# Performance work log

Measured on AMD Instinct MI355X. Metric: run time of the kernel, lower is better.

The kernel has to match this reference:

```python
import jax, jax.numpy as jnp
import numpy as np

T = 8192
D_IN = 512
D_QK = 64
D_V = 64


def setup_inputs() -> dict:
    key = jax.random.key(0)
    kx, kq, kk, kv, kl = jax.random.split(key, 5)
    x = jax.random.normal(kx, (T, D_IN), dtype=jnp.float32)
    Wq = jax.random.normal(kq, (D_IN, D_QK), dtype=jnp.float32) * 0.02
    Wk = jax.random.normal(kk, (D_IN, D_QK), dtype=jnp.float32) * 0.02
    Wv = jax.random.normal(kv, (D_IN, D_V), dtype=jnp.float32) * 0.02
    l = jax.random.normal(kl, (T, T), dtype=jnp.float32) * 0.02
    return {"x": x, "Wq": Wq, "Wk": Wk, "Wv": Wv, "l": l}


def reference(x, Wq, Wk, Wv, l):
    # q: [T, d_qk], k: [T, d_qk], v: [T, d_v]
    q = x @ Wq
    k = x @ Wk
    v = x @ Wv
    # scores: [T, S] = (q k^T) elementwise-weighted by learned tril matrix
    scores = jnp.einsum("tn,sn->ts", q, k) * jnp.tril(l)
    # output: [T, d_v]
    return scores @ v
```

## Files before the change

kernel.cpp:

```cpp
#include <hip/hip_runtime.h>
#include <hip/hip_bf16.h>

#define TT 8192
#define DIN 512
#define DQK 64

typedef __attribute__((ext_vector_type(8))) short short8;
typedef __attribute__((ext_vector_type(4))) float f32x4;

__global__ __launch_bounds__(256) void zero_kernel(float* __restrict__ out, int n4)
{
    int i = blockIdx.x * 256 + threadIdx.x;
    if (i < n4) ((f32x4*)out)[i] = (f32x4){0.f, 0.f, 0.f, 0.f};
}

__global__ __launch_bounds__(256) void wconv_kernel(
    const float* __restrict__ Wq, const float* __restrict__ Wk, const float* __restrict__ Wv,
    __hip_bfloat16* __restrict__ wtb)
{
    __shared__ float tile[64][65];
    const int m = blockIdx.y;
    const float* W = m == 0 ? Wq : (m == 1 ? Wk : Wv);
    const int k0 = blockIdx.x * 64;
    const int tid = threadIdx.x;

    {
        const int col4 = (tid & 15) * 4;
        #pragma unroll
        for (int it = 0; it < 4; ++it) {
            const int row = (tid >> 4) + it * 16;
            float4 v = *(const float4*)&W[(size_t)(k0 + row) * DQK + col4];
            tile[row][col4 + 0] = v.x; tile[row][col4 + 1] = v.y;
            tile[row][col4 + 2] = v.z; tile[row][col4 + 3] = v.w;
        }
    }
    __syncthreads();
    {
        const int d = tid >> 2;
        const int kc = (tid & 3) * 16;
        short tmp[16];
        #pragma unroll
        for (int j = 0; j < 16; ++j) {
            __hip_bfloat16 h = __float2bfloat16(tile[kc + j][d]);
            tmp[j] = *(short*)&h;
        }
        short* dst = (short*)wtb + ((size_t)m * 64 + d) * DIN + k0 + kc;
        *(short8*)dst       = *(short8*)&tmp[0];
        *(short8*)(dst + 8) = *(short8*)&tmp[8];
    }
}

#define PP 72

__global__ __launch_bounds__(256) void proj_kernel(
    const float* __restrict__ x,
    const __hip_bfloat16* __restrict__ wtb,
    __hip_bfloat16* __restrict__ qb, __hip_bfloat16* __restrict__ kb,
    __hip_bfloat16* __restrict__ vt)
{
    __shared__ short xb[64][PP];
    __shared__ short wb[3][64][PP];

    const int rowBase = blockIdx.x * 64;
    const int tid = threadIdx.x;
    const int lane = tid & 63;
    const int w = tid >> 6;
    const int lo = lane & 15, hi = lane >> 4;

    f32x4 acc[3][4];
    #pragma unroll
    for (int m = 0; m < 3; ++m)
        #pragma unroll
        for (int cf = 0; cf < 4; ++cf) acc[m][cf] = (f32x4){0.f, 0.f, 0.f, 0.f};

    for (int kk = 0; kk < DIN; kk += 64) {
        {
            const int r = tid >> 2;
            const int c0 = (tid & 3) * 16;
            const float* xp = x + (size_t)(rowBase + r) * DIN + kk + c0;
            short tmp[16];
            #pragma unroll
            for (int j = 0; j < 16; j += 4) {
                float4 v = *(const float4*)(xp + j);
                __hip_bfloat16 h0 = __float2bfloat16(v.x);
                __hip_bfloat16 h1 = __float2bfloat16(v.y);
                __hip_bfloat16 h2 = __float2bfloat16(v.z);
                __hip_bfloat16 h3 = __float2bfloat16(v.w);
                tmp[j + 0] = *(short*)&h0; tmp[j + 1] = *(short*)&h1;
                tmp[j + 2] = *(short*)&h2; tmp[j + 3] = *(short*)&h3;
            }
            *(short8*)&xb[r][c0]     = *(short8*)&tmp[0];
            *(short8*)&xb[r][c0 + 8] = *(short8*)&tmp[8];
        }
        {
            const int d = tid >> 2;
            const int kc = (tid & 3) * 16;
            #pragma unroll
            for (int m = 0; m < 3; ++m) {
                const short* src = (const short*)wtb + ((size_t)m * 64 + d) * DIN + kk + kc;
                *(short8*)&wb[m][d][kc]     = *(const short8*)src;
                *(short8*)&wb[m][d][kc + 8] = *(const short8*)(src + 8);
            }
        }
        __syncthreads();

        short8 a0 = *(short8*)&xb[w * 16 + lo][hi * 8];
        short8 a1 = *(short8*)&xb[w * 16 + lo][32 + hi * 8];
        #pragma unroll
        for (int m = 0; m < 3; ++m) {
            #pragma unroll
            for (int cf = 0; cf < 4; ++cf) {
                short8 b0 = *(short8*)&wb[m][cf * 16 + lo][hi * 8];
                short8 b1 = *(short8*)&wb[m][cf * 16 + lo][32 + hi * 8];
                acc[m][cf] = __builtin_amdgcn_mfma_f32_16x16x32_bf16(a0, b0, acc[m][cf], 0, 0, 0);
                acc[m][cf] = __builtin_amdgcn_mfma_f32_16x16x32_bf16(a1, b1, acc[m][cf], 0, 0, 0);
            }
        }
        __syncthreads();
    }

    #pragma unroll
    for (int cf = 0; cf < 4; ++cf) {
        #pragma unroll
        for (int r = 0; r < 4; ++r) {
            const int tg = rowBase + w * 16 + hi * 4 + r;
            const int d  = cf * 16 + lo;
            __hip_bfloat16 hq = __float2bfloat16(acc[0][cf][r]);
            __hip_bfloat16 hk = __float2bfloat16(acc[1][cf][r]);
            __hip_bfloat16 hv = __float2bfloat16(acc[2][cf][r]);
            qb[(size_t)tg * DQK + d] = hq;
            kb[(size_t)tg * DQK + d] = hk;
            vt[(size_t)d * TT + tg]  = hv;
        }
    }
}

#define TM 128
#define TS 64
#define SCHUNK 512
#define LP 72

__global__ __launch_bounds__(512) void attn_kernel(
    const __hip_bfloat16* __restrict__ qb,
    const __hip_bfloat16* __restrict__ kb,
    const __hip_bfloat16* __restrict__ vt,
    const float* __restrict__ l,
    float* __restrict__ out)
{
    __shared__ short K_lds[2][TS][LP];
    __shared__ short V_lds[2][DQK][LP];
    __shared__ short S_lds[8][16][LP];

    const int t0 = blockIdx.x * TM;
    const int sStart = blockIdx.y * SCHUNK;
    if (sStart >= t0 + TM) return;
    const int sEnd = min(sStart + SCHUNK, t0 + TM);

    const int tid = threadIdx.x;
    const int lane = tid & 63;
    const int w = tid >> 6;
    const int lo = lane & 15, hi = lane >> 4;
    const int trow = t0 + w * 16;
    const int r0 = hi * 4;

    const int srow = tid >> 3;
    const int sc8  = (tid & 7) * 8;

    short8 qf0, qf1;
    {
        const short* qp = (const short*)qb + (size_t)(trow + lo) * DQK;
        qf0 = *(const short8*)(qp + hi * 8);
        qf1 = *(const short8*)(qp + 32 + hi * 8);
    }

    f32x4 acc_o[4];
    #pragma unroll
    for (int i = 0; i < 4; ++i) acc_o[i] = (f32x4){0.f, 0.f, 0.f, 0.f};

    short8 kreg = *(const short8*)((const short*)kb + (size_t)(sStart + srow) * DQK + sc8);
    short8 vreg = *(const short8*)((const short*)vt + (size_t)srow * TT + sStart + sc8);

    float lvC[4][4];
    float lvN[4][4];
    {
        const bool act0 = (sStart <= trow + 15);
        #pragma unroll
        for (int sub = 0; sub < 4; ++sub) {
            const int s_glob = sStart + sub * 16 + lo;
            #pragma unroll
            for (int r = 0; r < 4; ++r) {
                const int tg = trow + r0 + r;
                lvC[sub][r] = (act0 && s_glob <= tg)
                    ? __builtin_nontemporal_load(&l[(size_t)tg * TT + s_glob]) : 0.f;
            }
        }
    }

    *(short8*)&K_lds[0][srow][sc8] = kreg;
    *(short8*)&V_lds[0][srow][sc8] = vreg;
    __syncthreads();

    int cur = 0;
    for (int s0 = sStart; s0 < sEnd; s0 += TS) {
        const int sN = s0 + TS;
        const bool havN = (sN < sEnd);

        if (havN) {
            kreg = *(const short8*)((const short*)kb + (size_t)(sN + srow) * DQK + sc8);
            vreg = *(const short8*)((const short*)vt + (size_t)srow * TT + sN + sc8);
        }

        const bool actN = havN && (sN <= trow + 15);
        if (actN) {
            if (sN + TS - 1 <= trow) {
                #pragma unroll
                for (int sub = 0; sub < 4; ++sub) {
                    const int s_glob = sN + sub * 16 + lo;
                    #pragma unroll
                    for (int r = 0; r < 4; ++r) {
                        const int tg = trow + r0 + r;
                        lvN[sub][r] = __builtin_nontemporal_load(&l[(size_t)tg * TT + s_glob]);
                    }
                }
            } else {
                #pragma unroll
                for (int sub = 0; sub < 4; ++sub) {
                    const int s_glob = sN + sub * 16 + lo;
                    #pragma unroll
                    for (int r = 0; r < 4; ++r) {
                        const int tg = trow + r0 + r;
                        lvN[sub][r] = (s_glob <= tg)
                            ? __builtin_nontemporal_load(&l[(size_t)tg * TT + s_glob]) : 0.f;
                    }
                }
            }
        } else {
            #pragma unroll
            for (int sub = 0; sub < 4; ++sub)
                #pragma unroll
                for (int r = 0; r < 4; ++r) lvN[sub][r] = 0.f;
        }

        if (s0 <= trow + 15) {
            #pragma unroll
            for (int sub = 0; sub < 4; ++sub) {
                f32x4 acc = (f32x4){0.f, 0.f, 0.f, 0.f};
                short8 b0 = *(short8*)&K_lds[cur][sub * 16 + lo][hi * 8];
                short8 b1 = *(short8*)&K_lds[cur][sub * 16 + lo][32 + hi * 8];
                acc = __builtin_amdgcn_mfma_f32_16x16x32_bf16(qf0, b0, acc, 0, 0, 0);
                acc = __builtin_amdgcn_mfma_f32_16x16x32_bf16(qf1, b1, acc, 0, 0, 0);
                #pragma unroll
                for (int r = 0; r < 4; ++r) {
                    float sv = acc[r] * lvC[sub][r];
                    __hip_bfloat16 h = __float2bfloat16(sv);
                    S_lds[w][r0 + r][sub * 16 + lo] = *(short*)&h;
                }
            }
            short8 a0 = *(short8*)&S_lds[w][lo][hi * 8];
            short8 a1 = *(short8*)&S_lds[w][lo][32 + hi * 8];
            #pragma unroll
            for (int ds = 0; ds < 4; ++ds) {
                short8 b0 = *(short8*)&V_lds[cur][ds * 16 + lo][hi * 8];
                short8 b1 = *(short8*)&V_lds[cur][ds * 16 + lo][32 + hi * 8];
                acc_o[ds] = __builtin_amdgcn_mfma_f32_16x16x32_bf16(a0, b0, acc_o[ds], 0, 0, 0);
                acc_o[ds] = __builtin_amdgcn_mfma_f32_16x16x32_bf16(a1, b1, acc_o[ds], 0, 0, 0);
            }
        }

        if (havN) {
            *(short8*)&K_lds[cur ^ 1][srow][sc8] = kreg;
            *(short8*)&V_lds[cur ^ 1][srow][sc8] = vreg;
        }
        __syncthreads();
        cur ^= 1;

        #pragma unroll
        for (int sub = 0; sub < 4; ++sub)
            #pragma unroll
            for (int r = 0; r < 4; ++r)
                lvC[sub][r] = lvN[sub][r];
    }

    #pragma unroll
    for (int ds = 0; ds < 4; ++ds) {
        #pragma unroll
        for (int r = 0; r < 4; ++r) {
            const int tg = trow + r0 + r;
            atomicAdd(&out[(size_t)tg * DQK + ds * 16 + lo], acc_o[ds][r]);
        }
    }
}

extern "C" void kernel_launch(void* const* d_in, const int* in_sizes, int n_in,
                              void* d_out, int out_size, void* d_ws, size_t ws_size,
                              hipStream_t stream) {
    const float* x  = (const float*)d_in[0];
    const float* Wq = (const float*)d_in[1];
    const float* Wk = (const float*)d_in[2];
    const float* Wv = (const float*)d_in[3];
    const float* l  = (const float*)d_in[4];
    float* out = (float*)d_out;

    __hip_bfloat16* qb  = (__hip_bfloat16*)d_ws;
    __hip_bfloat16* kb  = qb + (size_t)TT * DQK;
    __hip_bfloat16* vt  = kb + (size_t)TT * DQK;
    __hip_bfloat16* wtb = vt + (size_t)TT * DQK;

    zero_kernel<<<(out_size / 4 + 255) / 256, 256, 0, stream>>>(out, out_size / 4);
    wconv_kernel<<<dim3(DIN / 64, 3), 256, 0, stream>>>(Wq, Wk, Wv, wtb);
    proj_kernel<<<TT / 64, 256, 0, stream>>>(x, wtb, qb, kb, vt);
    attn_kernel<<<dim3(TT / TM, TT / SCHUNK), 512, 0, stream>>>(qb, kb, vt, l, out);
}
```

Baseline: 82.52 us.

## Vectorize l loads via transposed score MFMA, shuffle scores, rework projection

New measurement: 108.5 us. +31.5%, slower.

```diff
diff --git a/kernel.cpp b/kernel.cpp
--- a/kernel.cpp
+++ b/kernel.cpp
@@ -7,6 +7,25 @@
 
 typedef __attribute__((ext_vector_type(8))) short short8;
 typedef __attribute__((ext_vector_type(4))) float f32x4;
+typedef __attribute__((ext_vector_type(4))) unsigned u32x4;
+
+union S8U4 { u32x4 u; short8 s; };
+
+static __device__ __forceinline__ unsigned pack_bf16(float a, float b) {
+    __hip_bfloat16 ha = __float2bfloat16(a);
+    __hip_bfloat16 hb = __float2bfloat16(b);
+    return (unsigned)(*(unsigned short*)&ha) | ((unsigned)(*(unsigned short*)&hb) << 16);
+}
+
+static __device__ __forceinline__ short8 cvt8(const float* p) {
+    short tmp[8];
+    #pragma unroll
+    for (int j = 0; j < 8; ++j) {
+        __hip_bfloat16 h = __float2bfloat16(p[j]);
+        tmp[j] = *(short*)&h;
+    }
+    return *(short8*)tmp;
+}
 
 __global__ __launch_bounds__(256) void zero_kernel(float* __restrict__ out, int n4)
 {
@@ -50,21 +69,15 @@
     }
 }
 
-#define PP 72
-
-__global__ __launch_bounds__(256) void proj_kernel(
+__global__ __launch_bounds__(64) void proj_kernel(
     const float* __restrict__ x,
     const __hip_bfloat16* __restrict__ wtb,
     __hip_bfloat16* __restrict__ qb, __hip_bfloat16* __restrict__ kb,
     __hip_bfloat16* __restrict__ vt)
 {
-    __shared__ short xb[64][PP];
-    __shared__ short wb[3][64][PP];
-
-    const int rowBase = blockIdx.x * 64;
-    const int tid = threadIdx.x;
-    const int lane = tid & 63;
-    const int w = tid >> 6;
+    __shared__ float tile[16][65];
+    const int rowBase = blockIdx.x * 16;
+    const int lane = threadIdx.x;
     const int lo = lane & 15, hi = lane >> 4;
 
     f32x4 acc[3][4];
@@ -73,71 +86,63 @@
         #pragma unroll
         for (int cf = 0; cf < 4; ++cf) acc[m][cf] = (f32x4){0.f, 0.f, 0.f, 0.f};
 
+    const float* xp0 = x + (size_t)(rowBase + lo) * DIN + hi * 8;
+    const short* wb0 = (const short*)wtb + (size_t)lo * DIN + hi * 8;
+
     for (int kk = 0; kk < DIN; kk += 64) {
-        {
-            const int r = tid >> 2;
-            const int c0 = (tid & 3) * 16;
-            const float* xp = x + (size_t)(rowBase + r) * DIN + kk + c0;
-            short tmp[16];
-            #pragma unroll
-            for (int j = 0; j < 16; j += 4) {
-                float4 v = *(const float4*)(xp + j);
-                __hip_bfloat16 h0 = __float2bfloat16(v.x);
-                __hip_bfloat16 h1 = __float2bfloat16(v.y);
-                __hip_bfloat16 h2 = __float2bfloat16(v.z);
-                __hip_bfloat16 h3 = __float2bfloat16(v.w);
-                tmp[j + 0] = *(short*)&h0; tmp[j + 1] = *(short*)&h1;
-                tmp[j + 2] = *(short*)&h2; tmp[j + 3] = *(short*)&h3;
-            }
-            *(short8*)&xb[r][c0]     = *(short8*)&tmp[0];
-            *(short8*)&xb[r][c0 + 8] = *(short8*)&tmp[8];
-        }
-        {
-            const int d = tid >> 2;
-            const int kc = (tid & 3) * 16;
-            #pragma unroll
-            for (int m = 0; m < 3; ++m) {
-                const short* src = (const short*)wtb + ((size_t)m * 64 + d) * DIN + kk + kc;
-                *(short8*)&wb[m][d][kc]     = *(const short8*)src;
-                *(short8*)&wb[m][d][kc + 8] = *(const short8*)(src + 8);
-            }
-        }
-        __syncthreads();
-
-        short8 a0 = *(short8*)&xb[w * 16 + lo][hi * 8];
-        short8 a1 = *(short8*)&xb[w * 16 + lo][32 + hi * 8];
+        float xa[8], xb[8];
+        *(float4*)&xa[0] = *(const float4*)(xp0 + kk);
+        *(float4*)&xa[4] = *(const float4*)(xp0 + kk + 4);
+        *(float4*)&xb[0] = *(const float4*)(xp0 + kk + 32);
+        *(float4*)&xb[4] = *(const float4*)(xp0 + kk + 36);
+        short8 af0 = cvt8(xa), af1 = cvt8(xb);
         #pragma unroll
         for (int m = 0; m < 3; ++m) {
             #pragma unroll
             for (int cf = 0; cf < 4; ++cf) {
-                short8 b0 = *(short8*)&wb[m][cf * 16 + lo][hi * 8];
-                short8 b1 = *(short8*)&wb[m][cf * 16 + lo][32 + hi * 8];
-                acc[m][cf] = __builtin_amdgcn_mfma_f32_16x16x32_bf16(a0, b0, acc[m][cf], 0, 0, 0);
-                acc[m][cf] = __builtin_amdgcn_mfma_f32_16x16x32_bf16(a1, b1, acc[m][cf], 0, 0, 0);
-            }
-        }
-        __syncthreads();
-    }
-
-    #pragma unroll
-    for (int cf = 0; cf < 4; ++cf) {
-        #pragma unroll
-        for (int r = 0; r < 4; ++r) {
-            const int tg = rowBase + w * 16 + hi * 4 + r;
-            const int d  = cf * 16 + lo;
-            __hip_bfloat16 hq = __float2bfloat16(acc[0][cf][r]);
-            __hip_bfloat16 hk = __float2bfloat16(acc[1][cf][r]);
-            __hip_bfloat16 hv = __float2bfloat16(acc[2][cf][r]);
-            qb[(size_t)tg * DQK + d] = hq;
-            kb[(size_t)tg * DQK + d] = hk;
-            vt[(size_t)d * TT + tg]  = hv;
-        }
+                const short* wp = wb0 + ((size_t)m * 64 + cf * 16) * DIN + kk;
+                short8 b0 = *(const short8*)wp;
+                short8 b1 = *(const short8*)(wp + 32);
+                acc[m][cf] = __builtin_amdgcn_mfma_f32_16x16x32_bf16(af0, b0, acc[m][cf], 0, 0, 0);
+                acc[m][cf] = __builtin_amdgcn_mfma_f32_16x16x32_bf16(af1, b1, acc[m][cf], 0, 0, 0);
+            }
+        }
+    }
+
+    #pragma unroll
+    for (int m = 0; m < 2; ++m) {
+        __hip_bfloat16* o = (m == 0) ? qb : kb;
+        #pragma unroll
+        for (int cf = 0; cf < 4; ++cf)
+            #pragma unroll
+            for (int r = 0; r < 4; ++r)
+                o[(size_t)(rowBase + 4 * hi + r) * DQK + cf * 16 + lo] =
+                    __float2bfloat16(acc[m][cf][r]);
+    }
+
+    #pragma unroll
+    for (int cf = 0; cf < 4; ++cf)
+        #pragma unroll
+        for (int r = 0; r < 4; ++r)
+            tile[4 * hi + r][cf * 16 + lo] = acc[2][cf][r];
+    __syncthreads();
+    {
+        const int d = lane;
+        short tmp[16];
+        #pragma unroll
+        for (int j = 0; j < 16; ++j) {
+            __hip_bfloat16 h = __float2bfloat16(tile[j][d]);
+            tmp[j] = *(short*)&h;
+        }
+        short* dst = (short*)vt + (size_t)d * TT + rowBase;
+        *(short8*)dst       = *(short8*)&tmp[0];
+        *(short8*)(dst + 8) = *(short8*)&tmp[8];
     }
 }
 
 #define TM 128
 #define TS 64
-#define SCHUNK 512
+#define SCHUNK 256
 #define LP 72
 
 __global__ __launch_bounds__(512) void attn_kernel(
@@ -149,7 +154,6 @@
 {
     __shared__ short K_lds[2][TS][LP];
     __shared__ short V_lds[2][DQK][LP];
-    __shared__ short S_lds[8][16][LP];
 
     const int t0 = blockIdx.x * TM;
     const int sStart = blockIdx.y * SCHUNK;
@@ -161,14 +165,14 @@
     const int w = tid >> 6;
     const int lo = lane & 15, hi = lane >> 4;
     const int trow = t0 + w * 16;
-    const int r0 = hi * 4;
+    const int tmine = trow + lo;
 
     const int srow = tid >> 3;
     const int sc8  = (tid & 7) * 8;
 
     short8 qf0, qf1;
     {
-        const short* qp = (const short*)qb + (size_t)(trow + lo) * DQK;
+        const short* qp = (const short*)qb + (size_t)tmine * DQK;
         qf0 = *(const short8*)(qp + hi * 8);
         qf1 = *(const short8*)(qp + 32 + hi * 8);
     }
@@ -177,22 +181,29 @@
     #pragma unroll
     for (int i = 0; i < 4; ++i) acc_o[i] = (f32x4){0.f, 0.f, 0.f, 0.f};
 
+    const float* lrow = l + (size_t)tmine * TT;
+
     short8 kreg = *(const short8*)((const short*)kb + (size_t)(sStart + srow) * DQK + sc8);
     short8 vreg = *(const short8*)((const short*)vt + (size_t)srow * TT + sStart + sc8);
 
     float lvC[4][4];
-    float lvN[4][4];
-    {
-        const bool act0 = (sStart <= trow + 15);
-        #pragma unroll
-        for (int sub = 0; sub < 4; ++sub) {
-            const int s_glob = sStart + sub * 16 + lo;
-            #pragma unroll
-            for (int r = 0; r < 4; ++r) {
-                const int tg = trow + r0 + r;
-                lvC[sub][r] = (act0 && s_glob <= tg)
-                    ? __builtin_nontemporal_load(&l[(size_t)tg * TT + s_glob]) : 0.f;
-            }
+    if (sStart <= trow + 15) {
+        float raw[4][4];
+        #pragma unroll
+        for (int sub = 0; sub < 4; ++sub)
+            *(f32x4*)raw[sub] = __builtin_nontemporal_load(
+                (const f32x4*)(lrow + sStart + sub * 16 + 4 * hi));
+        if (sStart + 63 <= trow) {
+            #pragma unroll
+            for (int sub = 0; sub < 4; ++sub)
+                #pragma unroll
+                for (int r = 0; r < 4; ++r) lvC[sub][r] = raw[sub][r];
+        } else {
+            #pragma unroll
+            for (int sub = 0; sub < 4; ++sub)
+                #pragma unroll
+                for (int r = 0; r < 4; ++r)
+                    lvC[sub][r] = (sStart + sub * 16 + 4 * hi + r <= tmine) ? raw[sub][r] : 0.f;
         }
     }
 
@@ -200,70 +211,63 @@
     *(short8*)&V_lds[0][srow][sc8] = vreg;
     __syncthreads();
 
+    const int nsteps = (sEnd - sStart) / TS;
     int cur = 0;
-    for (int s0 = sStart; s0 < sEnd; s0 += TS) {
+    for (int n = 0; n < nsteps; ++n) {
+        const int s0 = sStart + n * TS;
         const int sN = s0 + TS;
-        const bool havN = (sN < sEnd);
-
+        const bool havN = (n + 1 < nsteps);
+        const bool actN = havN && (sN <= trow + 15);
+
+        float lvN[4][4];
+        if (actN) {
+            #pragma unroll
+            for (int sub = 0; sub < 4; ++sub)
+                *(f32x4*)lvN[sub] = __builtin_nontemporal_load(
+                    (const f32x4*)(lrow + sN + sub * 16 + 4 * hi));
+        }
         if (havN) {
             kreg = *(const short8*)((const short*)kb + (size_t)(sN + srow) * DQK + sc8);
             vreg = *(const short8*)((const short*)vt + (size_t)srow * TT + sN + sc8);
         }
 
-        const bool actN = havN && (sN <= trow + 15);
-        if (actN) {
-            if (sN + TS - 1 <= trow) {
-                #pragma unroll
-                for (int sub = 0; sub < 4; ++sub) {
-                    const int s_glob = sN + sub * 16 + lo;
-                    #pragma unroll
-                    for (int r = 0; r < 4; ++r) {
-                        const int tg = trow + r0 + r;
-                        lvN[sub][r] = __builtin_nontemporal_load(&l[(size_t)tg * TT + s_glob]);
-                    }
-                }
-            } else {
-                #pragma unroll
-                for (int sub = 0; sub < 4; ++sub) {
-                    const int s_glob = sN + sub * 16 + lo;
-                    #pragma unroll
-                    for (int r = 0; r < 4; ++r) {
-                        const int tg = trow + r0 + r;
-                        lvN[sub][r] = (s_glob <= tg)
-                            ? __builtin_nontemporal_load(&l[(size_t)tg * TT + s_glob]) : 0.f;
-                    }
-                }
-            }
-        } else {
-            #pragma unroll
-            for (int sub = 0; sub < 4; ++sub)
-                #pragma unroll
-                for (int r = 0; r < 4; ++r) lvN[sub][r] = 0.f;
-        }
-
         if (s0 <= trow + 15) {
+            unsigned pk[4][2];
             #pragma unroll
             for (int sub = 0; sub < 4; ++sub) {
-                f32x4 acc = (f32x4){0.f, 0.f, 0.f, 0.f};
                 short8 b0 = *(short8*)&K_lds[cur][sub * 16 + lo][hi * 8];
                 short8 b1 = *(short8*)&K_lds[cur][sub * 16 + lo][32 + hi * 8];
-                acc = __builtin_amdgcn_mfma_f32_16x16x32_bf16(qf0, b0, acc, 0, 0, 0);
-                acc = __builtin_amdgcn_mfma_f32_16x16x32_bf16(qf1, b1, acc, 0, 0, 0);
-                #pragma unroll
-                for (int r = 0; r < 4; ++r) {
-                    float sv = acc[r] * lvC[sub][r];
-                    __hip_bfloat16 h = __float2bfloat16(sv);
-                    S_lds[w][r0 + r][sub * 16 + lo] = *(short*)&h;
+                f32x4 a = (f32x4){0.f, 0.f, 0.f, 0.f};
+                a = __builtin_amdgcn_mfma_f32_16x16x32_bf16(b0, qf0, a, 0, 0, 0);
+                a = __builtin_amdgcn_mfma_f32_16x16x32_bf16(b1, qf1, a, 0, 0, 0);
+                pk[sub][0] = pack_bf16(a[0] * lvC[sub][0], a[1] * lvC[sub][1]);
+                pk[sub][1] = pack_bf16(a[2] * lvC[sub][2], a[3] * lvC[sub][3]);
+            }
+            const int srcA = lo | ((lane & 16) << 1);
+            unsigned a0dw[4], a1dw[4];
+            #pragma unroll
+            for (int h = 0; h < 2; ++h) {
+                const int src = srcA + 16 * h;
+                #pragma unroll
+                for (int p = 0; p < 2; ++p) {
+                    unsigned u0 = (unsigned)__shfl((int)pk[0][p], src, 64);
+                    unsigned u1 = (unsigned)__shfl((int)pk[1][p], src, 64);
+                    unsigned u2 = (unsigned)__shfl((int)pk[2][p], src, 64);
+                    unsigned u3 = (unsigned)__shfl((int)pk[3][p], src, 64);
+                    a0dw[2 * h + p] = (hi < 2) ? u0 : u1;
+                    a1dw[2 * h + p] = (hi < 2) ? u2 : u3;
                 }
             }
-            short8 a0 = *(short8*)&S_lds[w][lo][hi * 8];
-            short8 a1 = *(short8*)&S_lds[w][lo][32 + hi * 8];
+            S8U4 A0, A1;
+            A0.u = (u32x4){a0dw[0], a0dw[1], a0dw[2], a0dw[3]};
+            A1.u = (u32x4){a1dw[0], a1dw[1], a1dw[2], a1dw[3]};
+
             #pragma unroll
             for (int ds = 0; ds < 4; ++ds) {
                 short8 b0 = *(short8*)&V_lds[cur][ds * 16 + lo][hi * 8];
                 short8 b1 = *(short8*)&V_lds[cur][ds * 16 + lo][32 + hi * 8];
-                acc_o[ds] = __builtin_amdgcn_mfma_f32_16x16x32_bf16(a0, b0, acc_o[ds], 0, 0, 0);
-                acc_o[ds] = __builtin_amdgcn_mfma_f32_16x16x32_bf16(a1, b1, acc_o[ds], 0, 0, 0);
+                acc_o[ds] = __builtin_amdgcn_mfma_f32_16x16x32_bf16(A0.s, b0, acc_o[ds], 0, 0, 0);
+                acc_o[ds] = __builtin_amdgcn_mfma_f32_16x16x32_bf16(A1.s, b1, acc_o[ds], 0, 0, 0);
             }
         }
 
@@ -274,19 +278,30 @@
         __syncthreads();
         cur ^= 1;
 
-        #pragma unroll
-        for (int sub = 0; sub < 4; ++sub)
-            #pragma unroll
-            for (int r = 0; r < 4; ++r)
-                lvC[sub][r] = lvN[sub][r];
-    }
-
-    #pragma unroll
-    for (int ds = 0; ds < 4; ++ds) {
-        #pragma unroll
-        for (int r = 0; r < 4; ++r) {
-            const int tg = trow + r0 + r;
-            atomicAdd(&out[(size_t)tg * DQK + ds * 16 + lo], acc_o[ds][r]);
+        if (actN) {
+            if (sN + 63 <= trow) {
+                #pragma unroll
+                for (int sub = 0; sub < 4; ++sub)
+                    #pragma unroll
+                    for (int r = 0; r < 4; ++r) lvC[sub][r] = lvN[sub][r];
+            } else {
+                #pragma unroll
+                for (int sub = 0; sub < 4; ++sub)
+                    #pragma unroll
+                    for (int r = 0; r < 4; ++r)
+                        lvC[sub][r] = (sN + sub * 16 + 4 * hi + r <= tmine) ? lvN[sub][r] : 0.f;
+            }
+        }
+    }
+
+    if (sStart <= trow + 15) {
+        #pragma unroll
+        for (int ds = 0; ds < 4; ++ds) {
+            #pragma unroll
+            for (int r = 0; r < 4; ++r) {
+                const int tg = trow + 4 * hi + r;
+                atomicAdd(&out[(size_t)tg * DQK + ds * 16 + lo], acc_o[ds][r]);
+            }
         }
     }
 }
@@ -308,6 +323,6 @@
 
     zero_kernel<<<(out_size / 4 + 255) / 256, 256, 0, stream>>>(out, out_size / 4);
     wconv_kernel<<<dim3(DIN / 64, 3), 256, 0, stream>>>(Wq, Wk, Wv, wtb);
-    proj_kernel<<<TT / 64, 256, 0, stream>>>(x, wtb, qb, kb, vt);
+    proj_kernel<<<TT / 16, 64, 0, stream>>>(x, wtb, qb, kb, vt);
     attn_kernel<<<dim3(TT / TM, TT / SCHUNK), 512, 0, stream>>>(qb, kb, vt, l, out);
 }
```
